# Optimization experiments

Measured on AMD Instinct MI355X. Metric: run time of the kernel, lower is better.

The kernel has to match this reference:

```python
import jax, jax.numpy as jnp
import numpy as np

N_NODES = 100000
HIDDEN = 128
N_LAYERS = 3
N_EDGES = 600000


def setup_inputs() -> dict:
    key = jax.random.key(0)
    k_e, k_emb, k_w = jax.random.split(key, 3)
    edge_index = jax.random.randint(k_e, (2, N_EDGES), 0, N_NODES, dtype=jnp.int64 if jax.config.read('jax_enable_x64') else jnp.int32)
    embedding = jax.random.normal(k_emb, (N_NODES, HIDDEN), dtype=jnp.float32)
    Ws = jax.random.normal(k_w, (N_LAYERS, HIDDEN, HIDDEN), dtype=jnp.float32) * (1.0 / np.sqrt(HIDDEN))
    bs = jnp.zeros((N_LAYERS, HIDDEN), dtype=jnp.float32)
    return {"edge_index": edge_index, "embedding": embedding, "Ws": Ws, "bs": bs}


def _gcn_forward(embedding, Ws, bs, edge_index):
    N = embedding.shape[0]
    # PyG GCNConv default: add self-loops, symmetric deg^{-1/2} normalization
    loop = jnp.arange(N, dtype=edge_index.dtype)
    src = jnp.concatenate([edge_index[0], loop])  # [E+N]
    dst = jnp.concatenate([edge_index[1], loop])
    deg = jax.ops.segment_sum(jnp.ones_like(dst, dtype=embedding.dtype), dst, num_segments=N)
    dinv = jnp.where(deg > 0, jax.lax.rsqrt(jnp.where(deg > 0, deg, 1.0)), 0.0)
    norm = dinv[src] * dinv[dst]  # [E+N]

    x = embedding
    for l in range(Ws.shape[0]):
        h = x @ Ws[l]                              # [N, d] linear transform
        msg = h[src] * norm[:, None]               # gather + scale
        x = jax.ops.segment_sum(msg, dst, num_segments=N) + bs[l]  # scatter-add
        x = jax.nn.relu(x)
        # dropout is identity in eval mode
    return x


def reference(edge_index, embedding, Ws, bs):
    return _gcn_forward(embedding, Ws, bs, edge_index)
```

## Files before the change

kernel.cpp:

```cpp
#include <hip/hip_runtime.h>
#include <hip/hip_bf16.h>


#define HID 128

typedef __attribute__((ext_vector_type(8))) short short8;
typedef __attribute__((ext_vector_type(4))) float floatx4;

#define WLDS 136


__global__ void k_init_cnt(int* cnt, int n) {
    int i = blockIdx.x * blockDim.x + threadIdx.x;
    if (i < n) cnt[i] = 1;
}

__global__ void k_count_edges(const int* __restrict__ ei, int* cnt, int E) {
    int e = blockIdx.x * blockDim.x + threadIdx.x;
    if (e < E) atomicAdd(&cnt[ei[E + e]], 1);
}

__global__ void k_scanA(const int* __restrict__ cnt, int* csum, int n) {
    __shared__ int sd[256];
    int t = threadIdx.x;
    int base = blockIdx.x * 1024 + t * 4;
    int s = 0;
#pragma unroll
    for (int j = 0; j < 4; j++) { int i = base + j; if (i < n) s += cnt[i]; }
    sd[t] = s; __syncthreads();
    for (int off = 128; off > 0; off >>= 1) {
        if (t < off) sd[t] += sd[t + off];
        __syncthreads();
    }
    if (t == 0) csum[blockIdx.x] = sd[0];
}

__global__ void k_scanB(int* csum, int* offsets, int nchunk, int n) {
    __shared__ int sd[256];
    int t = threadIdx.x;
    int v = (t < nchunk) ? csum[t] : 0;
    sd[t] = v; __syncthreads();
    for (int off = 1; off < 256; off <<= 1) {
        int u = (t >= off) ? sd[t - off] : 0;
        __syncthreads();
        sd[t] += u;
        __syncthreads();
    }
    if (t < nchunk) csum[t] = sd[t] - v;
    if (t == 0) offsets[n] = sd[255];
}

__global__ void k_scanC(const int* __restrict__ cnt, const int* __restrict__ csum,
                        int* offsets, int* cursor, float* dinv,
                        int2* adj, int n) {
    __shared__ int sd[256];
    int t = threadIdx.x;
    int base = blockIdx.x * 1024 + t * 4;
    int c[4]; int s = 0;
#pragma unroll
    for (int j = 0; j < 4; j++) {
        c[j] = (base + j < n) ? cnt[base + j] : 0;
        s += c[j];
    }
    sd[t] = s; __syncthreads();
    for (int off = 1; off < 256; off <<= 1) {
        int v = (t >= off) ? sd[t - off] : 0;
        __syncthreads();
        sd[t] += v;
        __syncthreads();
    }
    int run = sd[t] - s + csum[blockIdx.x];
#pragma unroll
    for (int j = 0; j < 4; j++) {
        int i = base + j;
        if (i < n) {
            offsets[i] = run;
            float di = rsqrtf((float)c[j]);
            dinv[i] = di;
            cursor[i] = run + 1;
            adj[run] = make_int2(i, __float_as_int(di * di));
        }
        run += c[j];
    }
}

__global__ void k_fill_edges(const int* __restrict__ ei, int* cursor,
                             const float* __restrict__ dinv,
                             int2* adj, int E) {
    int e = blockIdx.x * blockDim.x + threadIdx.x;
    if (e >= E) return;
    int s = ei[e];
    int d = ei[E + e];
    int pos = atomicAdd(&cursor[d], 1);
    adj[pos] = make_int2(s, __float_as_int(dinv[s] * dinv[d]));
}

__global__ void k_packW(const float* __restrict__ Ws, ushort* Whp, ushort* Wlp,
                        int nlayers) {
    int idx = blockIdx.x * blockDim.x + threadIdx.x;
    if (idx >= nlayers * HID * HID) return;
    int l = idx >> 14;
    int n = (idx >> 7) & 127;
    int k = idx & 127;
    float w = Ws[(size_t)l * HID * HID + k * HID + n];
    __hip_bfloat16 hi = __float2bfloat16(w);
    float lo = w - __bfloat162float(hi);
    __hip_bfloat16 lo16 = __float2bfloat16(lo);
    Whp[idx] = *(ushort*)&hi;
    Wlp[idx] = *(ushort*)&lo16;
}


__global__ __launch_bounds__(256) void k_agg(const float* __restrict__ x,
                                             const int* __restrict__ offsets,
                                             const int2* __restrict__ adj,
                                             ushort* __restrict__ yh,
                                             ushort* __restrict__ yl, int n) {
    int gid = blockIdx.x * blockDim.x + threadIdx.x;
    int lane = gid & 63;
    int q    = lane >> 4;
    int ql   = lane & 15;
    int f4   = (q & 1) * 16 + ql;
    int epar = q >> 1;
    int nwaves = (gridDim.x * blockDim.x) >> 6;

    int node0 = gid >> 6;
    int nbeg = 0, nend = 0;
    if (node0 < n) { nbeg = offsets[node0]; nend = offsets[node0 + 1]; }

    for (int node = node0; node < n; node += nwaves) {
        int beg = nbeg;
        int end = nend;
        int nxt = node + nwaves;
        if (nxt < n) { nbeg = offsets[nxt]; nend = offsets[nxt + 1]; }

        float4 acc = {0.f, 0.f, 0.f, 0.f};

        int e0 = beg + epar;
        int c0 = e0 < end ? e0 : end - 1;
        int2 a0 = adj[c0];
        int e1 = e0 + 2;
        int c1 = e1 < end ? e1 : end - 1;
        int2 a1 = adj[c1];
        int e2 = e0 + 4;
        int c2 = e2 < end ? e2 : end - 1;
        int2 a2 = adj[c2];
        float w0 = e0 < end ? __int_as_float(a0.y) : 0.f;
        float w1 = e1 < end ? __int_as_float(a1.y) : 0.f;
        float w2 = e2 < end ? __int_as_float(a2.y) : 0.f;
        float4 v0 = ((const float4*)(x + (size_t)a0.x * HID))[f4];
        float4 v1 = ((const float4*)(x + (size_t)a1.x * HID))[f4];
        int s2 = a2.x;

        for (int e = beg + 4; e < end; e += 2) {
            int e3 = e + 2 + epar;
            int c3 = e3 < end ? e3 : end - 1;
            int2 a3 = adj[c3];
            float w3 = e3 < end ? __int_as_float(a3.y) : 0.f;

            float4 v2 = ((const float4*)(x + (size_t)s2 * HID))[f4];

            acc.x += w0 * v0.x;
            acc.y += w0 * v0.y;
            acc.z += w0 * v0.z;
            acc.w += w0 * v0.w;

            v0 = v1; v1 = v2;
            w0 = w1; w1 = w2; w2 = w3;
            s2 = a3.x;
        }
        acc.x += w0 * v0.x;
        acc.y += w0 * v0.y;
        acc.z += w0 * v0.z;
        acc.w += w0 * v0.w;
        acc.x += w1 * v1.x;
        acc.y += w1 * v1.y;
        acc.z += w1 * v1.z;
        acc.w += w1 * v1.w;

        acc.x += __shfl_xor(acc.x, 32);
        acc.y += __shfl_xor(acc.y, 32);
        acc.z += __shfl_xor(acc.z, 32);
        acc.w += __shfl_xor(acc.w, 32);
        if (lane < 32) {
            float a[4] = {acc.x, acc.y, acc.z, acc.w};
            ushort4 h, l;
            ushort* hp = (ushort*)&h;
            ushort* lp = (ushort*)&l;
#pragma unroll
            for (int j = 0; j < 4; j++) {
                __hip_bfloat16 hi = __float2bfloat16(a[j]);
                float lo = a[j] - __bfloat162float(hi);
                __hip_bfloat16 lo16 = __float2bfloat16(lo);
                hp[j] = *(ushort*)&hi;
                lp[j] = *(ushort*)&lo16;
            }
            ((ushort4*)(yh + (size_t)node * HID))[lane] = h;
            ((ushort4*)(yl + (size_t)node * HID))[lane] = l;
        }
    }
}


__global__ __launch_bounds__(256, 2) void k_gemm_mfma(const ushort* __restrict__ yh,
                                                      const ushort* __restrict__ yl,
                                                      const ushort* __restrict__ Whp,
                                                      const ushort* __restrict__ Wlp,
                                                      const float* __restrict__ bias,
                                                      float* __restrict__ out, int n) {
    __shared__ ushort Wh_lds[HID * WLDS];
    __shared__ ushort Wl_lds[HID * WLDS];
    int t = threadIdx.x;
    int wave = t >> 6;
    int lane = t & 63;
    int m16  = lane & 15;
    int oct  = lane >> 4;

    short8 ah[2][4], al[2][4];
#pragma unroll
    for (int mt = 0; mt < 2; mt++) {
        int rowA = blockIdx.x * 128 + wave * 32 + mt * 16 + m16;
        const ushort* hb = yh + (size_t)rowA * HID + oct * 8;
        const ushort* lb = yl + (size_t)rowA * HID + oct * 8;
#pragma unroll
        for (int ks = 0; ks < 4; ks++) {
            ah[mt][ks] = *(const short8*)(hb + ks * 32);
            al[mt][ks] = *(const short8*)(lb + ks * 32);
        }
    }

    for (int idx = t; idx < HID * 16; idx += 256) {
        int r = idx >> 4, c8 = idx & 15;
        ((uint4*)(Wh_lds + r * WLDS))[c8] = ((const uint4*)(Whp + r * HID))[c8];
        ((uint4*)(Wl_lds + r * WLDS))[c8] = ((const uint4*)(Wlp + r * HID))[c8];
    }
    __syncthreads();

    floatx4 acc0[8], acc1[8];
#pragma unroll
    for (int c = 0; c < 8; c++) {
        acc0[c] = (floatx4){0.f, 0.f, 0.f, 0.f};
        acc1[c] = (floatx4){0.f, 0.f, 0.f, 0.f};
    }

#pragma unroll
    for (int ks = 0; ks < 4; ks++) {
#pragma unroll
        for (int c = 0; c < 8; c++) {
            const ushort* bp = Wh_lds + (c * 16 + m16) * WLDS + ks * 32 + oct * 8;
            const ushort* bq = Wl_lds + (c * 16 + m16) * WLDS + ks * 32 + oct * 8;
            short8 bh = *(const short8*)bp;
            short8 bl = *(const short8*)bq;
            acc0[c] = __builtin_amdgcn_mfma_f32_16x16x32_bf16(ah[0][ks], bh, acc0[c], 0, 0, 0);
            acc0[c] = __builtin_amdgcn_mfma_f32_16x16x32_bf16(ah[0][ks], bl, acc0[c], 0, 0, 0);
            acc0[c] = __builtin_amdgcn_mfma_f32_16x16x32_bf16(al[0][ks], bh, acc0[c], 0, 0, 0);
            acc1[c] = __builtin_amdgcn_mfma_f32_16x16x32_bf16(ah[1][ks], bh, acc1[c], 0, 0, 0);
            acc1[c] = __builtin_amdgcn_mfma_f32_16x16x32_bf16(ah[1][ks], bl, acc1[c], 0, 0, 0);
            acc1[c] = __builtin_amdgcn_mfma_f32_16x16x32_bf16(al[1][ks], bh, acc1[c], 0, 0, 0);
        }
    }

#pragma unroll
    for (int mt = 0; mt < 2; mt++) {
        int rowbase = blockIdx.x * 128 + wave * 32 + mt * 16 + oct * 4;
#pragma unroll
        for (int c = 0; c < 8; c++) {
            int col = c * 16 + m16;
            float b = bias[col];
            floatx4 a = mt == 0 ? acc0[c] : acc1[c];
#pragma unroll
            for (int r = 0; r < 4; r++) {
                int row = rowbase + r;
                if (row < n) {
                    float v = fmaxf(a[r] + b, 0.f);
                    out[(size_t)row * HID + col] = v;
                }
            }
        }
    }
}


extern "C" void kernel_launch(void* const* d_in, const int* in_sizes, int n_in,
                              void* d_out, int out_size, void* d_ws, size_t ws_size,
                              hipStream_t stream) {
    const int* ei = (const int*)d_in[0];
    const float* emb = (const float*)d_in[1];
    const float* Ws = (const float*)d_in[2];
    const float* bs = (const float*)d_in[3];

    const int E = in_sizes[0] / 2;
    const int N = in_sizes[1] / HID;
    const int NL = in_sizes[3] / HID;
    const int TOT = E + N;
    const int NPAD = ((N + 127) / 128) * 128;

    char* p = (char*)d_ws;
    auto carve = [&](size_t bytes) {
        char* r = p;
        p += (bytes + 255) & ~(size_t)255;
        return (void*)r;
    };
    int*    cnt      = (int*)   carve((size_t)N * 4);
    int*    offsets  = (int*)   carve((size_t)(N + 1) * 4);
    int*    cursor   = (int*)   carve((size_t)N * 4);
    float*  dinv     = (float*) carve((size_t)N * 4);
    int*    csum     = (int*)   carve(1024 * 4);
    int2*   adj      = (int2*)  carve((size_t)TOT * 8);
    ushort* yh       = (ushort*)carve((size_t)NPAD * HID * 2);
    ushort* yl       = (ushort*)carve((size_t)NPAD * HID * 2);
    ushort* Whp      = (ushort*)carve((size_t)NL * HID * HID * 2);
    ushort* Wlp      = (ushort*)carve((size_t)NL * HID * HID * 2);
    float*  xbufA    = (float*) carve((size_t)N * HID * 4);
    float*  xbufB    = (float*) d_out;

    const int NCHUNK = (N + 1023) / 1024;

    k_init_cnt<<<(N + 255) / 256, 256, 0, stream>>>(cnt, N);
    k_count_edges<<<(E + 255) / 256, 256, 0, stream>>>(ei, cnt, E);
    k_scanA<<<NCHUNK, 256, 0, stream>>>(cnt, csum, N);
    k_scanB<<<1, 256, 0, stream>>>(csum, offsets, NCHUNK, N);
    k_scanC<<<NCHUNK, 256, 0, stream>>>(cnt, csum, offsets, cursor, dinv,
                                        adj, N);
    k_fill_edges<<<(E + 255) / 256, 256, 0, stream>>>(ei, cursor, dinv,
                                                      adj, E);
    k_packW<<<(NL * HID * HID + 255) / 256, 256, 0, stream>>>(Ws, Whp, Wlp, NL);

    const int aggBlocks = 2048;
    const int gemmBlocks = NPAD / 128;
    const float* x = emb;
    for (int l = 0; l < NL; l++) {
        float* o = (l == 1) ? xbufA : xbufB;
        k_agg<<<aggBlocks, 256, 0, stream>>>(x, offsets, adj, yh, yl, N);
        k_gemm_mfma<<<gemmBlocks, 256, 0, stream>>>(yh, yl,
                                                    Whp + (size_t)l * HID * HID,
                                                    Wlp + (size_t)l * HID * HID,
                                                    bs + (size_t)l * HID, o, N);
        x = o;
    }
}
```

Before: 435.0 us.

## Fuse CSR preprocessing kernels into one persistent kernel with grid barriers

Merges cnt init, weight packing, edge counting, and the three-stage scan into a single 512-block persistent kernel separated by software grid barriers, replacing six launches with a memset plus one launch. Edge counting also reads destination indices as int4. The aim is to cut launch overhead and inter-kernel gaps in the preprocessing phase. It relies on all 512 blocks being co-resident, otherwise the spin barriers deadlock, and the atomic spin waits add their own latency.

```diff
diff --git a/kernel.cpp b/kernel.cpp
--- a/kernel.cpp
+++ b/kernel.cpp
@@ -10,77 +10,122 @@
 #define WLDS 136
 
 
-__global__ void k_init_cnt(int* cnt, int n) {
-    int i = blockIdx.x * blockDim.x + threadIdx.x;
-    if (i < n) cnt[i] = 1;
-}
-
-__global__ void k_count_edges(const int* __restrict__ ei, int* cnt, int E) {
-    int e = blockIdx.x * blockDim.x + threadIdx.x;
-    if (e < E) atomicAdd(&cnt[ei[E + e]], 1);
-}
-
-__global__ void k_scanA(const int* __restrict__ cnt, int* csum, int n) {
+__device__ __forceinline__ void grid_barrier(int* bar, int phase, int nblk) {
+    __syncthreads();
+    if (threadIdx.x == 0) {
+        __threadfence();
+        int ticket = atomicAdd(&bar[0], 1);
+        if (ticket == (phase + 1) * nblk - 1) {
+            atomicExch(&bar[1], phase + 1);
+        } else {
+            while (atomicAdd(&bar[1], 0) < phase + 1) {
+                __builtin_amdgcn_s_sleep(8);
+            }
+        }
+        __threadfence();
+    }
+    __syncthreads();
+}
+
+__global__ __launch_bounds__(256) void k_pre(const int* __restrict__ ei,
+                                             const float* __restrict__ Ws,
+                                             int* cnt, int* csum, int* offsets,
+                                             int* cursor, float* dinv, int2* adj,
+                                             ushort* Whp, ushort* Wlp, int* bar,
+                                             int n, int E, int nlayers, int nchunk) {
+    const int NT = gridDim.x * blockDim.x;
+    const int tid = blockIdx.x * blockDim.x + threadIdx.x;
+    const int nblk = gridDim.x;
+
+    for (int i = tid; i < n; i += NT) cnt[i] = 1;
+    for (int idx = tid; idx < nlayers * HID * HID; idx += NT) {
+        int l = idx >> 14;
+        int nn = (idx >> 7) & 127;
+        int k = idx & 127;
+        float w = Ws[(size_t)l * HID * HID + k * HID + nn];
+        __hip_bfloat16 hi = __float2bfloat16(w);
+        float lo = w - __bfloat162float(hi);
+        __hip_bfloat16 lo16 = __float2bfloat16(lo);
+        Whp[idx] = *(ushort*)&hi;
+        Wlp[idx] = *(ushort*)&lo16;
+    }
+    grid_barrier(bar, 0, nblk);
+
+    {
+        const int4* d4 = (const int4*)(ei + E);
+        int quads = E >> 2;
+        for (int qd = tid; qd < quads; qd += NT) {
+            int4 d = d4[qd];
+            atomicAdd(&cnt[d.x], 1);
+            atomicAdd(&cnt[d.y], 1);
+            atomicAdd(&cnt[d.z], 1);
+            atomicAdd(&cnt[d.w], 1);
+        }
+        for (int e = (quads << 2) + tid; e < E; e += NT)
+            atomicAdd(&cnt[ei[E + e]], 1);
+    }
+    grid_barrier(bar, 1, nblk);
+
     __shared__ int sd[256];
     int t = threadIdx.x;
-    int base = blockIdx.x * 1024 + t * 4;
-    int s = 0;
-#pragma unroll
-    for (int j = 0; j < 4; j++) { int i = base + j; if (i < n) s += cnt[i]; }
-    sd[t] = s; __syncthreads();
-    for (int off = 128; off > 0; off >>= 1) {
-        if (t < off) sd[t] += sd[t + off];
+
+    if (blockIdx.x < nchunk) {
+        int base = blockIdx.x * 1024 + t * 4;
+        int s = 0;
+#pragma unroll
+        for (int j = 0; j < 4; j++) { int i = base + j; if (i < n) s += cnt[i]; }
+        sd[t] = s; __syncthreads();
+        for (int off = 128; off > 0; off >>= 1) {
+            if (t < off) sd[t] += sd[t + off];
+            __syncthreads();
+        }
+        if (t == 0) csum[blockIdx.x] = sd[0];
+    }
+    grid_barrier(bar, 2, nblk);
+
+    if (blockIdx.x < nchunk) {
+        __shared__ int cb_sh, tot_sh;
+        int v = (t < nchunk) ? csum[t] : 0;
+        sd[t] = v; __syncthreads();
+        for (int off = 1; off < 256; off <<= 1) {
+            int u = (t >= off) ? sd[t - off] : 0;
+            __syncthreads();
+            sd[t] += u;
+            __syncthreads();
+        }
+        if (t == blockIdx.x) cb_sh = sd[t] - v;
+        if (t == nchunk - 1) tot_sh = sd[t];
         __syncthreads();
-    }
-    if (t == 0) csum[blockIdx.x] = sd[0];
-}
-
-__global__ void k_scanB(int* csum, int* offsets, int nchunk, int n) {
-    __shared__ int sd[256];
-    int t = threadIdx.x;
-    int v = (t < nchunk) ? csum[t] : 0;
-    sd[t] = v; __syncthreads();
-    for (int off = 1; off < 256; off <<= 1) {
-        int u = (t >= off) ? sd[t - off] : 0;
-        __syncthreads();
-        sd[t] += u;
-        __syncthreads();
-    }
-    if (t < nchunk) csum[t] = sd[t] - v;
-    if (t == 0) offsets[n] = sd[255];
-}
-
-__global__ void k_scanC(const int* __restrict__ cnt, const int* __restrict__ csum,
-                        int* offsets, int* cursor, float* dinv,
-                        int2* adj, int n) {
-    __shared__ int sd[256];
-    int t = threadIdx.x;
-    int base = blockIdx.x * 1024 + t * 4;
-    int c[4]; int s = 0;
-#pragma unroll
-    for (int j = 0; j < 4; j++) {
-        c[j] = (base + j < n) ? cnt[base + j] : 0;
-        s += c[j];
-    }
-    sd[t] = s; __syncthreads();
-    for (int off = 1; off < 256; off <<= 1) {
-        int v = (t >= off) ? sd[t - off] : 0;
-        __syncthreads();
-        sd[t] += v;
-        __syncthreads();
-    }
-    int run = sd[t] - s + csum[blockIdx.x];
-#pragma unroll
-    for (int j = 0; j < 4; j++) {
-        int i = base + j;
-        if (i < n) {
-            offsets[i] = run;
-            float di = rsqrtf((float)c[j]);
-            dinv[i] = di;
-            cursor[i] = run + 1;
-            adj[run] = make_int2(i, __float_as_int(di * di));
-        }
-        run += c[j];
+        if (blockIdx.x == 0 && t == 0) offsets[n] = tot_sh;
+        int chunkbase = cb_sh;
+
+        int base = blockIdx.x * 1024 + t * 4;
+        int c[4]; int s = 0;
+#pragma unroll
+        for (int j = 0; j < 4; j++) {
+            c[j] = (base + j < n) ? cnt[base + j] : 0;
+            s += c[j];
+        }
+        sd[t] = s; __syncthreads();
+        for (int off = 1; off < 256; off <<= 1) {
+            int vv = (t >= off) ? sd[t - off] : 0;
+            __syncthreads();
+            sd[t] += vv;
+            __syncthreads();
+        }
+        int run = sd[t] - s + chunkbase;
+#pragma unroll
+        for (int j = 0; j < 4; j++) {
+            int i = base + j;
+            if (i < n) {
+                offsets[i] = run;
+                float di = rsqrtf((float)c[j]);
+                dinv[i] = di;
+                cursor[i] = run + 1;
+                adj[run] = make_int2(i, __float_as_int(di * di));
+            }
+            run += c[j];
+        }
     }
 }
 
@@ -93,21 +138,6 @@
     int d = ei[E + e];
     int pos = atomicAdd(&cursor[d], 1);
     adj[pos] = make_int2(s, __float_as_int(dinv[s] * dinv[d]));
-}
-
-__global__ void k_packW(const float* __restrict__ Ws, ushort* Whp, ushort* Wlp,
-                        int nlayers) {
-    int idx = blockIdx.x * blockDim.x + threadIdx.x;
-    if (idx >= nlayers * HID * HID) return;
-    int l = idx >> 14;
-    int n = (idx >> 7) & 127;
-    int k = idx & 127;
-    float w = Ws[(size_t)l * HID * HID + k * HID + n];
-    __hip_bfloat16 hi = __float2bfloat16(w);
-    float lo = w - __bfloat162float(hi);
-    __hip_bfloat16 lo16 = __float2bfloat16(lo);
-    Whp[idx] = *(ushort*)&hi;
-    Wlp[idx] = *(ushort*)&lo16;
 }
 
 
@@ -301,6 +331,7 @@
         p += (bytes + 255) & ~(size_t)255;
         return (void*)r;
     };
+    int*    bar      = (int*)   carve(256);
     int*    cnt      = (int*)   carve((size_t)N * 4);
     int*    offsets  = (int*)   carve((size_t)(N + 1) * 4);
     int*    cursor   = (int*)   carve((size_t)N * 4);
@@ -316,15 +347,10 @@
 
     const int NCHUNK = (N + 1023) / 1024;
 
-    k_init_cnt<<<(N + 255) / 256, 256, 0, stream>>>(cnt, N);
-    k_count_edges<<<(E + 255) / 256, 256, 0, stream>>>(ei, cnt, E);
-    k_scanA<<<NCHUNK, 256, 0, stream>>>(cnt, csum, N);
-    k_scanB<<<1, 256, 0, stream>>>(csum, offsets, NCHUNK, N);
-    k_scanC<<<NCHUNK, 256, 0, stream>>>(cnt, csum, offsets, cursor, dinv,
-                                        adj, N);
-    k_fill_edges<<<(E + 255) / 256, 256, 0, stream>>>(ei, cursor, dinv,
-                                                      adj, E);
-    k_packW<<<(NL * HID * HID + 255) / 256, 256, 0, stream>>>(Ws, Whp, Wlp, NL);
+    hipMemsetAsync(bar, 0, 16, stream);
+    k_pre<<<512, 256, 0, stream>>>(ei, Ws, cnt, csum, offsets, cursor, dinv,
+                                   adj, Whp, Wlp, bar, N, E, NL, NCHUNK);
+    k_fill_edges<<<(E + 255) / 256, 256, 0, stream>>>(ei, cursor, dinv, adj, E);
 
     const int aggBlocks = 2048;
     const int gemmBlocks = NPAD / 128;
```

After: 546.9 us. 25.7% more time.

## Fuse aggregation and MFMA GEMM into one kernel via LDS staging

Applied to the files above, without the earlier changes.

Merges the sparse aggregation kernel and the split-bf16 MFMA GEMM into one 512-thread kernel per 128-row tile. Aggregated rows are written to LDS as hi/lo bf16 instead of going to global yh/yl buffers, and W is prefetched into registers during aggregation. This removes the global round trip of the intermediate and one launch per layer. In exchange it uses about 136KB of LDS, so only one block fits per CU, and grid-stride load balancing gives way to a fixed 16 nodes per wave.

```diff
diff --git a/kernel.cpp b/kernel.cpp
--- a/kernel.cpp
+++ b/kernel.cpp
@@ -111,27 +111,46 @@
 }
 
 
-__global__ __launch_bounds__(256) void k_agg(const float* __restrict__ x,
-                                             const int* __restrict__ offsets,
-                                             const int2* __restrict__ adj,
-                                             ushort* __restrict__ yh,
-                                             ushort* __restrict__ yl, int n) {
-    int gid = blockIdx.x * blockDim.x + threadIdx.x;
-    int lane = gid & 63;
+__global__ __launch_bounds__(512, 1) void k_agg_gemm(const float* __restrict__ x,
+                                                     const int* __restrict__ offsets,
+                                                     const int2* __restrict__ adj,
+                                                     const ushort* __restrict__ Whp,
+                                                     const ushort* __restrict__ Wlp,
+                                                     const float* __restrict__ bias,
+                                                     float* __restrict__ out, int n) {
+    __shared__ ushort Wh_lds[HID * WLDS];
+    __shared__ ushort Wl_lds[HID * WLDS];
+    __shared__ ushort Yh_lds[HID * WLDS];
+    __shared__ ushort Yl_lds[HID * WLDS];
+
+    int t = threadIdx.x;
+    int wid  = t >> 6;
+    int lane = t & 63;
+    int tb = blockIdx.x * 128;
+
+    uint4 wreg_h[4], wreg_l[4];
+#pragma unroll
+    for (int j = 0; j < 4; j++) {
+        int idx = t + j * 512;
+        int r = idx >> 4, c8 = idx & 15;
+        wreg_h[j] = ((const uint4*)(Whp + r * HID))[c8];
+        wreg_l[j] = ((const uint4*)(Wlp + r * HID))[c8];
+    }
+
     int q    = lane >> 4;
     int ql   = lane & 15;
     int f4   = (q & 1) * 16 + ql;
     int epar = q >> 1;
-    int nwaves = (gridDim.x * blockDim.x) >> 6;
-
-    int node0 = gid >> 6;
+
+    int node = tb + wid;
     int nbeg = 0, nend = 0;
-    if (node0 < n) { nbeg = offsets[node0]; nend = offsets[node0 + 1]; }
-
-    for (int node = node0; node < n; node += nwaves) {
+    if (node < n) { nbeg = offsets[node]; nend = offsets[node + 1]; }
+
+    for (int i = 0; i < 16; i++, node += 8) {
+        if (node >= n) break;
         int beg = nbeg;
         int end = nend;
-        int nxt = node + nwaves;
+        int nxt = node + 8;
         if (nxt < n) { nbeg = offsets[nxt]; nend = offsets[nxt + 1]; }
 
         float4 acc = {0.f, 0.f, 0.f, 0.f};
@@ -195,53 +214,36 @@
                 hp[j] = *(ushort*)&hi;
                 lp[j] = *(ushort*)&lo16;
             }
-            ((ushort4*)(yh + (size_t)node * HID))[lane] = h;
-            ((ushort4*)(yl + (size_t)node * HID))[lane] = l;
-        }
-    }
-}
-
-
-__global__ __launch_bounds__(256, 2) void k_gemm_mfma(const ushort* __restrict__ yh,
-                                                      const ushort* __restrict__ yl,
-                                                      const ushort* __restrict__ Whp,
-                                                      const ushort* __restrict__ Wlp,
-                                                      const float* __restrict__ bias,
-                                                      float* __restrict__ out, int n) {
-    __shared__ ushort Wh_lds[HID * WLDS];
-    __shared__ ushort Wl_lds[HID * WLDS];
-    int t = threadIdx.x;
-    int wave = t >> 6;
-    int lane = t & 63;
-    int m16  = lane & 15;
-    int oct  = lane >> 4;
-
-    short8 ah[2][4], al[2][4];
-#pragma unroll
-    for (int mt = 0; mt < 2; mt++) {
-        int rowA = blockIdx.x * 128 + wave * 32 + mt * 16 + m16;
-        const ushort* hb = yh + (size_t)rowA * HID + oct * 8;
-        const ushort* lb = yl + (size_t)rowA * HID + oct * 8;
-#pragma unroll
-        for (int ks = 0; ks < 4; ks++) {
-            ah[mt][ks] = *(const short8*)(hb + ks * 32);
-            al[mt][ks] = *(const short8*)(lb + ks * 32);
-        }
-    }
-
-    for (int idx = t; idx < HID * 16; idx += 256) {
+            int lr = node - tb;
+            ((ushort4*)(Yh_lds + (size_t)lr * WLDS))[lane] = h;
+            ((ushort4*)(Yl_lds + (size_t)lr * WLDS))[lane] = l;
+        }
+    }
+
+#pragma unroll
+    for (int j = 0; j < 4; j++) {
+        int idx = t + j * 512;
         int r = idx >> 4, c8 = idx & 15;
-        ((uint4*)(Wh_lds + r * WLDS))[c8] = ((const uint4*)(Whp + r * HID))[c8];
-        ((uint4*)(Wl_lds + r * WLDS))[c8] = ((const uint4*)(Wlp + r * HID))[c8];
+        ((uint4*)(Wh_lds + r * WLDS))[c8] = wreg_h[j];
+        ((uint4*)(Wl_lds + r * WLDS))[c8] = wreg_l[j];
     }
     __syncthreads();
 
-    floatx4 acc0[8], acc1[8];
-#pragma unroll
-    for (int c = 0; c < 8; c++) {
-        acc0[c] = (floatx4){0.f, 0.f, 0.f, 0.f};
-        acc1[c] = (floatx4){0.f, 0.f, 0.f, 0.f};
-    }
+    int m16 = lane & 15;
+    int oct = lane >> 4;
+
+    short8 ah[4], al[4];
+#pragma unroll
+    for (int ks = 0; ks < 4; ks++) {
+        const ushort* hb = Yh_lds + (wid * 16 + m16) * WLDS + ks * 32 + oct * 8;
+        const ushort* lb = Yl_lds + (wid * 16 + m16) * WLDS + ks * 32 + oct * 8;
+        ah[ks] = *(const short8*)hb;
+        al[ks] = *(const short8*)lb;
+    }
+
+    floatx4 cacc[8];
+#pragma unroll
+    for (int c = 0; c < 8; c++) cacc[c] = (floatx4){0.f, 0.f, 0.f, 0.f};
 
 #pragma unroll
     for (int ks = 0; ks < 4; ks++) {
@@ -251,30 +253,23 @@
             const ushort* bq = Wl_lds + (c * 16 + m16) * WLDS + ks * 32 + oct * 8;
             short8 bh = *(const short8*)bp;
             short8 bl = *(const short8*)bq;
-            acc0[c] = __builtin_amdgcn_mfma_f32_16x16x32_bf16(ah[0][ks], bh, acc0[c], 0, 0, 0);
-            acc0[c] = __builtin_amdgcn_mfma_f32_16x16x32_bf16(ah[0][ks], bl, acc0[c], 0, 0, 0);
-            acc0[c] = __builtin_amdgcn_mfma_f32_16x16x32_bf16(al[0][ks], bh, acc0[c], 0, 0, 0);
-            acc1[c] = __builtin_amdgcn_mfma_f32_16x16x32_bf16(ah[1][ks], bh, acc1[c], 0, 0, 0);
-            acc1[c] = __builtin_amdgcn_mfma_f32_16x16x32_bf16(ah[1][ks], bl, acc1[c], 0, 0, 0);
-            acc1[c] = __builtin_amdgcn_mfma_f32_16x16x32_bf16(al[1][ks], bh, acc1[c], 0, 0, 0);
-        }
-    }
-
-#pragma unroll
-    for (int mt = 0; mt < 2; mt++) {
-        int rowbase = blockIdx.x * 128 + wave * 32 + mt * 16 + oct * 4;
-#pragma unroll
-        for (int c = 0; c < 8; c++) {
-            int col = c * 16 + m16;
-            float b = bias[col];
-            floatx4 a = mt == 0 ? acc0[c] : acc1[c];
-#pragma unroll
-            for (int r = 0; r < 4; r++) {
-                int row = rowbase + r;
-                if (row < n) {
-                    float v = fmaxf(a[r] + b, 0.f);
-                    out[(size_t)row * HID + col] = v;
-                }
+            cacc[c] = __builtin_amdgcn_mfma_f32_16x16x32_bf16(ah[ks], bh, cacc[c], 0, 0, 0);
+            cacc[c] = __builtin_amdgcn_mfma_f32_16x16x32_bf16(ah[ks], bl, cacc[c], 0, 0, 0);
+            cacc[c] = __builtin_amdgcn_mfma_f32_16x16x32_bf16(al[ks], bh, cacc[c], 0, 0, 0);
+        }
+    }
+
+    int rowbase = tb + wid * 16 + oct * 4;
+#pragma unroll
+    for (int c = 0; c < 8; c++) {
+        int col = c * 16 + m16;
+        float b = bias[col];
+#pragma unroll
+        for (int r = 0; r < 4; r++) {
+            int row = rowbase + r;
+            if (row < n) {
+                float v = fmaxf(cacc[c][r] + b, 0.f);
+                out[(size_t)row * HID + col] = v;
             }
         }
     }
@@ -307,8 +302,6 @@
     float*  dinv     = (float*) carve((size_t)N * 4);
     int*    csum     = (int*)   carve(1024 * 4);
     int2*   adj      = (int2*)  carve((size_t)TOT * 8);
-    ushort* yh       = (ushort*)carve((size_t)NPAD * HID * 2);
-    ushort* yl       = (ushort*)carve((size_t)NPAD * HID * 2);
     ushort* Whp      = (ushort*)carve((size_t)NL * HID * HID * 2);
     ushort* Wlp      = (ushort*)carve((size_t)NL * HID * HID * 2);
     float*  xbufA    = (float*) carve((size_t)N * HID * 4);
@@ -326,13 +319,11 @@
                                                       adj, E);
     k_packW<<<(NL * HID * HID + 255) / 256, 256, 0, stream>>>(Ws, Whp, Wlp, NL);
 
-    const int aggBlocks = 2048;
-    const int gemmBlocks = NPAD / 128;
+    const int fusedBlocks = NPAD / 128;
     const float* x = emb;
     for (int l = 0; l < NL; l++) {
         float* o = (l == 1) ? xbufA : xbufB;
-        k_agg<<<aggBlocks, 256, 0, stream>>>(x, offsets, adj, yh, yl, N);
-        k_gemm_mfma<<<gemmBlocks, 256, 0, stream>>>(yh, yl,
+        k_agg_gemm<<<fusedBlocks, 512, 0, stream>>>(x, offsets, adj,
                                                     Whp + (size_t)l * HID * HID,
                                                     Wlp + (size_t)l * HID * HID,
                                                     bs + (size_t)l * HID, o, N);
```

Result: slower. 545.6 us (+25.4%).
